# Kernel optimization log

Measured on AMD Instinct MI355X. Metric: run time of the kernel, lower is better.

The kernel has to match this reference:

```python
import jax, jax.numpy as jnp
import numpy as np

N = 50000
E = 800000
IN_C, HID, OUT_C, DEPTH, HEADS = 3, 128, 64, 4, 4
EPS = 1e-6
NEG_SLOPE = 0.2  # PyG GATConv default leaky_relu slope


def setup_inputs() -> dict:
    key = jax.random.key(0)
    ks = jax.random.split(key, 12)
    x = jax.random.normal(ks[0], (N, IN_C), dtype=jnp.float32)
    edge_index = jax.random.randint(ks[1], (2, E), 0, N, dtype=jnp.int32)
    s = 0.05
    return {
        "x": x,
        "edge_index": edge_index,
        "W_in": jax.random.normal(ks[2], (IN_C, HID), dtype=jnp.float32) * s,
        "b_in": jnp.zeros((HID,), jnp.float32),
        # per-layer GATConv params, stacked over depth
        "W_conv": jax.random.normal(ks[3], (DEPTH, HID, HEADS * HID), dtype=jnp.float32) * s,
        "att_src": jax.random.normal(ks[4], (DEPTH, HEADS, HID), dtype=jnp.float32) * s,
        "att_dst": jax.random.normal(ks[5], (DEPTH, HEADS, HID), dtype=jnp.float32) * s,
        "b_conv": jnp.zeros((DEPTH, HID), jnp.float32),
        "ln_gamma": jnp.ones((DEPTH, HID), jnp.float32),
        "ln_beta": jnp.zeros((DEPTH, HID), jnp.float32),
        "W_out": jax.random.normal(ks[6], (HID, OUT_C), dtype=jnp.float32) * s,
        "b_out": jnp.zeros((OUT_C,), jnp.float32),
    }


def _layer_norm(x, gamma, beta):
    mu = jnp.mean(x, axis=-1, keepdims=True)
    var = jnp.mean(jnp.square(x - mu), axis=-1, keepdims=True)
    return (x - mu) * jax.lax.rsqrt(var + EPS) * gamma + beta


def _gat_conv(x, src, dst, W, a_src, a_dst, bias):
    # x: [N, HID]; src/dst: [E2] (self-loops already appended)
    xh = (x @ W).reshape(N, HEADS, HID)                       # [N, H, C]
    alpha_s = jnp.einsum("nhc,hc->nh", xh, a_src)             # [N, H]
    alpha_d = jnp.einsum("nhc,hc->nh", xh, a_dst)             # [N, H]
    e = jax.nn.leaky_relu(alpha_s[src] + alpha_d[dst], NEG_SLOPE)  # [E2, H]
    # segment softmax over incoming edges of each destination node
    m = jax.ops.segment_max(e, dst, num_segments=N)           # [N, H]
    p = jnp.exp(e - m[dst])                                   # [E2, H]
    z = jax.ops.segment_sum(p, dst, num_segments=N)           # [N, H]
    alpha = p / z[dst]                                        # [E2, H]
    msg = alpha[:, :, None] * xh[src]                         # [E2, H, C]
    out = jax.ops.segment_sum(msg, dst, num_segments=N)       # [N, H, C]
    # concat=False -> mean over heads, then bias
    return out.mean(axis=1) + bias


def reference(x, edge_index, W_in, b_in, W_conv, att_src, att_dst, b_conv,
              ln_gamma, ln_beta, W_out, b_out):
    # add self-loops (PyG GATConv default add_self_loops=True)
    loops = jnp.arange(N, dtype=edge_index.dtype)
    src = jnp.concatenate([edge_index[0], loops])
    dst = jnp.concatenate([edge_index[1], loops])

    h = x @ W_in + b_in
    for i in range(DEPTH):
        residual = h
        h = _layer_norm(h, ln_gamma[i], ln_beta[i])
        h = _gat_conv(h, src, dst, W_conv[i], att_src[i], att_dst[i], b_conv[i])
        h = jax.nn.relu(h)
        h = h + residual
    return h @ W_out + b_out
```

## Files before the change

### kernel.cpp

```cpp
#include <hip/hip_runtime.h>
#include <hip/hip_fp16.h>
#include <math.h>

#define N_NODES 50000
#define E_EDGES 800000
#define E2 (E_EDGES + N_NODES)
#define HID 128
#define HEADS 4
#define OUTC 64
#define DEPTH 4
#define NEG_SLOPE 0.2f
#define LN_EPS 1e-6f
#define NT2 3125
#define AROW 520

typedef float f32x4 __attribute__((ext_vector_type(4)));
typedef float f32x2 __attribute__((ext_vector_type(2)));
typedef _Float16 half8 __attribute__((ext_vector_type(8)));


__global__ void k_deg(const int* __restrict__ ei, int* __restrict__ deg) {
    int e = blockIdx.x * 256 + threadIdx.x;
    if (e >= E2) return;
    int d = (e < E_EDGES) ? ei[E_EDGES + e] : (e - E_EDGES);
    atomicAdd(&deg[d], 1);
}


__global__ __launch_bounds__(256) void k_hist(const int* __restrict__ deg,
                                              int* __restrict__ hist) {
    __shared__ int lh[256];
    int t = threadIdx.x;
    lh[t] = 0;
    __syncthreads();
    int base = blockIdx.x * 1024;
    #pragma unroll
    for (int i = 0; i < 4; ++i) {
        int n = base + t + i * 256;
        if (n < N_NODES) atomicAdd(&lh[min(deg[n], 255)], 1);
    }
    __syncthreads();
    if (lh[t]) atomicAdd(&hist[t], lh[t]);
}


__global__ void k_hscan(const int* __restrict__ hist, int* __restrict__ hcur,
                        int* __restrict__ nprefix, int* __restrict__ eprefix,
                        int* __restrict__ row_ptr) {
    __shared__ int sm[256], se[256];
    int t = threadIdx.x;
    int v = hist[t];
    sm[t] = v;
    se[t] = v * t;
    __syncthreads();
    for (int off = 1; off < 256; off <<= 1) {
        int u = (t >= off) ? sm[t - off] : 0;
        int w = (t >= off) ? se[t - off] : 0;
        __syncthreads();
        sm[t] += u;
        se[t] += w;
        __syncthreads();
    }
    int np = sm[t] - v;
    int ep = se[t] - v * t;
    hcur[t] = np;
    nprefix[t] = np;
    eprefix[t] = ep;
    if (t == 0) row_ptr[N_NODES] = E2;
}


__global__ __launch_bounds__(256) void k_permfill(const int* __restrict__ deg,
                                                  int* __restrict__ hcur,
                                                  const int* __restrict__ nprefix,
                                                  const int* __restrict__ eprefix,
                                                  int* __restrict__ perm,
                                                  int* __restrict__ inv,
                                                  int* __restrict__ row_ptr) {
    __shared__ int lh[256];
    __shared__ int lbase[256];
    int t = threadIdx.x;
    lh[t] = 0;
    __syncthreads();
    int base = blockIdx.x * 1024;
    int myb[4], myr[4];
    #pragma unroll
    for (int i = 0; i < 4; ++i) {
        int n = base + t + i * 256;
        if (n < N_NODES) {
            int b = min(deg[n], 255);
            myb[i] = b;
            myr[i] = atomicAdd(&lh[b], 1);
        } else myb[i] = -1;
    }
    __syncthreads();
    if (lh[t]) lbase[t] = atomicAdd(&hcur[t], lh[t]);
    __syncthreads();
    #pragma unroll
    for (int i = 0; i < 4; ++i) {
        if (myb[i] >= 0) {
            int n = base + t + i * 256;
            int b = myb[i];
            int pos = lbase[b] + myr[i];
            perm[pos] = n;
            inv[n] = pos;
            row_ptr[pos] = eprefix[b] + (pos - nprefix[b]) * b;
        }
    }
}

__global__ void k_fill(const int* __restrict__ ei, const int* __restrict__ row_ptr,
                       const int* __restrict__ inv, int* __restrict__ cur,
                       int* __restrict__ csr_src) {
    int e = blockIdx.x * 256 + threadIdx.x;
    if (e >= E2) return;
    int s, d;
    if (e < E_EDGES) { s = ei[e]; d = ei[E_EDGES + e]; } else { s = d = e - E_EDGES; }
    int nd = inv[d], ns = inv[s];
    int pos = atomicAdd(&cur[nd], 1);
    csr_src[row_ptr[nd] + pos] = ns;
}


__global__ void k_prep(const float* __restrict__ W_conv, const float* __restrict__ att_s,
                       const float* __restrict__ att_d, const float* __restrict__ W_out,
                       _Float16* __restrict__ Bp, float* __restrict__ ws_all,
                       _Float16* __restrict__ Bout) {
    int idx = blockIdx.x * 256 + threadIdx.x;
    if (idx < DEPTH * 65536) {
        int jj    = idx & 7;
        int lane  = (idx >> 3) & 63;
        int kc    = (idx >> 9) & 15;
        int ntile = (idx >> 13) & 7;
        int layer = idx >> 16;
        int k = kc * 32 + (lane >> 4) * 8 + jj;
        int n = ntile * 16 + (lane & 15);
        int hh = k >> 7;
        int s  = k & 127;
        int c  = (s & 7) * 16 + (s >> 3);
        Bp[idx] = (_Float16)(0.25f * W_conv[(size_t)layer * 65536 + (size_t)c * 512 + hh * HID + n]);
        return;
    }
    int i2 = idx - DEPTH * 65536;
    if (i2 < DEPTH * 1024) {
        int j = i2 & 7, c = (i2 >> 3) & 127, layer = i2 >> 10;
        int hh = j & 3, sd = j >> 2;
        const float* Wr = W_conv + (size_t)layer * 65536 + (size_t)c * 512 + hh * HID;
        const float* at = (sd ? att_d : att_s) + (size_t)layer * HEADS * HID + hh * HID;
        float s = 0.f;
        for (int cc = 0; cc < HID; ++cc) s += Wr[cc] * at[cc];
        ws_all[i2] = s;
        return;
    }
    int i3 = i2 - DEPTH * 1024;
    if (i3 < 8192) {
        int j    = i3 & 7;
        int lane = (i3 >> 3) & 63;
        int nt   = (i3 >> 9) & 3;
        int kc   = i3 >> 11;
        int k = kc * 32 + (lane >> 4) * 8 + j;
        int c = (k & 7) * 16 + (k >> 3);
        int n = nt * 16 + (lane & 15);
        Bout[i3] = (_Float16)W_out[(size_t)c * OUTC + n];
    }
}


__global__ __launch_bounds__(256) void k_in_proj_ln(const float* __restrict__ x,
                                                    const int* __restrict__ perm,
                                                    const float* __restrict__ W,
                                                    const float* __restrict__ bias,
                                                    const float* __restrict__ gamma,
                                                    const float* __restrict__ beta,
                                                    const float* __restrict__ ws,
                                                    float* __restrict__ h,
                                                    unsigned char* __restrict__ ln8,
                                                    float* __restrict__ as_,
                                                    float* __restrict__ ad_) {
    int tid = threadIdx.x;
    int lane = tid & 63;
    int nd = blockIdx.x * 4 + (tid >> 6);
    int orig = perm[nd];
    const float* xr = x + (size_t)orig * 3;
    float x0 = xr[0], x1 = xr[1], x2 = xr[2];
    int j0 = lane, j1 = lane + 64;
    float a = bias[j0] + x0 * W[j0] + x1 * W[HID + j0] + x2 * W[2 * HID + j0];
    float b = bias[j1] + x0 * W[j1] + x1 * W[HID + j1] + x2 * W[2 * HID + j1];
    size_t base = (size_t)nd * HID;
    h[base + j0] = a;
    h[base + j1] = b;
    float s = a + b;
    for (int o = 1; o < 64; o <<= 1) s += __shfl_xor(s, o);
    float mu = s * (1.0f / 128.0f);
    float da = a - mu, db = b - mu;
    float v = da * da + db * db;
    for (int o = 1; o < 64; o <<= 1) v += __shfl_xor(v, o);
    float rstd = rsqrtf(v * (1.0f / 128.0f) + LN_EPS);
    float va = da * rstd * gamma[j0] + beta[j0];
    float vb = db * rstd * gamma[j1] + beta[j1];

    float ap[8];
    for (int j = 0; j < 8; ++j)
        ap[j] = va * ws[j0 * 8 + j] + vb * ws[j1 * 8 + j];
    for (int o = 1; o < 64; o <<= 1)
        for (int j = 0; j < 8; ++j) ap[j] += __shfl_xor(ap[j], o);
    if (lane == 0) {
        for (int hh = 0; hh < 4; ++hh) {
            as_[nd * 4 + hh] = ap[hh];
            ad_[nd * 4 + hh] = ap[4 + hh];
        }
    }

    float pv[8];
    for (int t = 0; t < 8; ++t) {
        int c = t * 16 + (lane & 15);
        float s1 = __shfl(va, c & 63);
        float s2 = __shfl(vb, c & 63);
        pv[t] = (c < 64) ? s1 : s2;
    }
    if (lane < 16) {
        int w0 = __builtin_amdgcn_cvt_pk_fp8_f32(pv[0], pv[1], 0, false);
        w0     = __builtin_amdgcn_cvt_pk_fp8_f32(pv[2], pv[3], w0, true);
        int w1 = __builtin_amdgcn_cvt_pk_fp8_f32(pv[4], pv[5], 0, false);
        w1     = __builtin_amdgcn_cvt_pk_fp8_f32(pv[6], pv[7], w1, true);
        *(int2*)(ln8 + base + lane * 8) = make_int2(w0, w1);
    }
}


__global__ __launch_bounds__(256, 4) void k_layer(const unsigned char* __restrict__ ln8r,
                                               const int* __restrict__ row_ptr,
                                               const int* __restrict__ csr_src,
                                               const float* __restrict__ asr,
                                               const float* __restrict__ adr,
                                               const _Float16* __restrict__ Bp,
                                               const float* __restrict__ ws,
                                               const float* __restrict__ bias,
                                               const float* __restrict__ gamma,
                                               const float* __restrict__ beta,
                                               float* __restrict__ h,
                                               unsigned char* __restrict__ ln8w,
                                               float* __restrict__ asw,
                                               float* __restrict__ adw,
                                               _Float16* __restrict__ h16,
                                               int write_ln, int last) {
    __shared__ __align__(16) unsigned char smraw[16 * AROW * 2];
    _Float16* Afr = (_Float16*)smraw;
    float (*Cts)[132] = (float (*)[132])smraw;

    int tid  = threadIdx.x;
    int lane = tid & 63;
    int w    = tid >> 6;
    int g    = lane >> 4;
    int l    = lane & 15;
    int quad = lane >> 4;
    int l15  = lane & 15;
    int tile = NT2 - 1 - blockIdx.x;
    int m    = w * 4 + g;
    int nd   = tile * 16 + m;

    int e0 = row_ptr[nd], e1 = row_ptr[nd + 1];
    float4 ad4 = *(const float4*)(adr + (size_t)nd * 4);

    f32x2 a00 = (f32x2)(0.f), a01 = (f32x2)(0.f), a02 = (f32x2)(0.f), a03 = (f32x2)(0.f);
    f32x2 a10 = (f32x2)(0.f), a11 = (f32x2)(0.f), a12 = (f32x2)(0.f), a13 = (f32x2)(0.f);
    f32x2 a20 = (f32x2)(0.f), a21 = (f32x2)(0.f), a22 = (f32x2)(0.f), a23 = (f32x2)(0.f);
    f32x2 a30 = (f32x2)(0.f), a31 = (f32x2)(0.f), a32 = (f32x2)(0.f), a33 = (f32x2)(0.f);
    float4 zz = make_float4(0.f, 0.f, 0.f, 0.f);

    const unsigned char* xb = ln8r + l * 8;

#define EDGE_P(Q, P) do {                                                   \
    float t_;                                                               \
    t_ = (Q).x + ad4.x; t_ = (t_ >= 0.f) ? t_ : NEG_SLOPE * t_; (P).x = __expf(t_); \
    t_ = (Q).y + ad4.y; t_ = (t_ >= 0.f) ? t_ : NEG_SLOPE * t_; (P).y = __expf(t_); \
    t_ = (Q).z + ad4.z; t_ = (t_ >= 0.f) ? t_ : NEG_SLOPE * t_; (P).z = __expf(t_); \
    t_ = (Q).w + ad4.w; t_ = (t_ >= 0.f) ? t_ : NEG_SLOPE * t_; (P).w = __expf(t_); \
} while (0)

#define ACC_EDGE(P, X) do {                                                 \
    f32x2 v0 = __builtin_amdgcn_cvt_pk_f32_fp8((X).x, false);               \
    f32x2 v1 = __builtin_amdgcn_cvt_pk_f32_fp8((X).x, true);                \
    f32x2 v2 = __builtin_amdgcn_cvt_pk_f32_fp8((X).y, false);               \
    f32x2 v3 = __builtin_amdgcn_cvt_pk_f32_fp8((X).y, true);                \
    a00 += (f32x2)((P).x) * v0; a01 += (f32x2)((P).x) * v1;                 \
    a02 += (f32x2)((P).x) * v2; a03 += (f32x2)((P).x) * v3;                 \
    a10 += (f32x2)((P).y) * v0; a11 += (f32x2)((P).y) * v1;                 \
    a12 += (f32x2)((P).y) * v2; a13 += (f32x2)((P).y) * v3;                 \
    a20 += (f32x2)((P).z) * v0; a21 += (f32x2)((P).z) * v1;                 \
    a22 += (f32x2)((P).z) * v2; a23 += (f32x2)((P).z) * v3;                 \
    a30 += (f32x2)((P).w) * v0; a31 += (f32x2)((P).w) * v1;                 \
    a32 += (f32x2)((P).w) * v2; a33 += (f32x2)((P).w) * v3;                 \
    zz.x += (P).x; zz.y += (P).y; zz.z += (P).z; zz.w += (P).w;             \
} while (0)

    int e = e0;
    for (; e + 4 <= e1; e += 4) {
        int s0 = csr_src[e];
        int s1 = csr_src[e + 1];
        int s2 = csr_src[e + 2];
        int s3 = csr_src[e + 3];
        float4 q0 = *(const float4*)(asr + (size_t)s0 * 4);
        float4 q1 = *(const float4*)(asr + (size_t)s1 * 4);
        float4 q2 = *(const float4*)(asr + (size_t)s2 * 4);
        float4 q3 = *(const float4*)(asr + (size_t)s3 * 4);
        int2 x0 = *(const int2*)(xb + (size_t)s0 * 128);
        int2 x1 = *(const int2*)(xb + (size_t)s1 * 128);
        int2 x2 = *(const int2*)(xb + (size_t)s2 * 128);
        int2 x3 = *(const int2*)(xb + (size_t)s3 * 128);
        float4 p0, p1, p2, p3;
        EDGE_P(q0, p0);
        EDGE_P(q1, p1);
        EDGE_P(q2, p2);
        EDGE_P(q3, p3);
        ACC_EDGE(p0, x0);
        ACC_EDGE(p1, x1);
        ACC_EDGE(p2, x2);
        ACC_EDGE(p3, x3);
    }
    for (; e < e1; ++e) {
        int s0 = csr_src[e];
        float4 q0 = *(const float4*)(asr + (size_t)s0 * 4);
        int2 x0 = *(const int2*)(xb + (size_t)s0 * 128);
        float4 p0;
        EDGE_P(q0, p0);
        ACC_EDGE(p0, x0);
    }
#undef EDGE_P
#undef ACC_EDGE

    {
        f32x2 i0 = (f32x2)(1.0f / zz.x), i1 = (f32x2)(1.0f / zz.y);
        f32x2 i2 = (f32x2)(1.0f / zz.z), i3 = (f32x2)(1.0f / zz.w);
        a00 *= i0; a01 *= i0; a02 *= i0; a03 *= i0;
        a10 *= i1; a11 *= i1; a12 *= i1; a13 *= i1;
        a20 *= i2; a21 *= i2; a22 *= i2; a23 *= i2;
        a30 *= i3; a31 *= i3; a32 *= i3; a33 *= i3;
        _Float16* rowp = Afr + m * AROW + l15 * 8;
        union { _Float16 hx[8]; int4 v4; } cf;
#define STORE_HEAD(H, P0, P1, P2, P3) do {                                  \
        cf.hx[0] = (_Float16)P0[0]; cf.hx[1] = (_Float16)P0[1];             \
        cf.hx[2] = (_Float16)P1[0]; cf.hx[3] = (_Float16)P1[1];             \
        cf.hx[4] = (_Float16)P2[0]; cf.hx[5] = (_Float16)P2[1];             \
        cf.hx[6] = (_Float16)P3[0]; cf.hx[7] = (_Float16)P3[1];             \
        *(int4*)(rowp + (H) * 128) = cf.v4;                                 \
} while (0)
        STORE_HEAD(0, a00, a01, a02, a03);
        STORE_HEAD(1, a10, a11, a12, a13);
        STORE_HEAD(2, a20, a21, a22, a23);
        STORE_HEAD(3, a30, a31, a32, a33);
#undef STORE_HEAD
    }
    __syncthreads();

    f32x4 c0 = (f32x4)(0.f), c1 = (f32x4)(0.f);
    {
        int nt0 = w * 2, nt1 = w * 2 + 1;
        const _Float16* b0p = Bp + (size_t)nt0 * 8192 + lane * 8;
        const _Float16* b1p = Bp + (size_t)nt1 * 8192 + lane * 8;
        const _Float16* ar = Afr + (lane & 15) * AROW + (lane >> 4) * 8;
        #pragma unroll
        for (int kc = 0; kc < 16; ++kc) {
            half8 a  = *(const half8*)(ar + kc * 32);
            half8 b0 = *(const half8*)(b0p + kc * 512);
            half8 b1 = *(const half8*)(b1p + kc * 512);
            c0 = __builtin_amdgcn_mfma_f32_16x16x32_f16(a, b0, c0, 0, 0, 0);
            c1 = __builtin_amdgcn_mfma_f32_16x16x32_f16(a, b1, c1, 0, 0, 0);
        }
    }
    __syncthreads();
    {
        int nt0 = w * 2, nt1 = w * 2 + 1;
        #pragma unroll
        for (int r = 0; r < 4; ++r) {
            Cts[quad * 4 + r][nt0 * 16 + l15] = c0[r];
            Cts[quad * 4 + r][nt1 * 16 + l15] = c1[r];
        }
    }
    __syncthreads();

    int row = quad * 4 + w;
    int node = tile * 16 + row;
    float* hr = h + (size_t)node * HID;

    float rv[8];
    #pragma unroll
    for (int nt = 0; nt < 8; ++nt) {
        float t = Cts[row][nt * 16 + l15] + bias[nt * 16 + l15];
        t = fmaxf(t, 0.f);
        rv[nt] = t + hr[nt * 16 + l15];
    }
    if (!last) {
        #pragma unroll
        for (int nt = 0; nt < 8; ++nt) hr[nt * 16 + l15] = rv[nt];
    } else {
        union { _Float16 hx[8]; int4 v4; } cf;
        #pragma unroll
        for (int nt = 0; nt < 8; ++nt) cf.hx[nt] = (_Float16)rv[nt];
        int kc = l15 >> 2;
        int lf = (l15 & 3) * 16 + row;
        *(int4*)(h16 + (((size_t)tile * 4 + kc) * 64 + lf) * 8) = cf.v4;
    }

    if (write_ln) {
        float ga[8], be[8];
        f32x4 wsa[8], wsb[8];
        #pragma unroll
        for (int nt = 0; nt < 8; ++nt) {
            int c = nt * 16 + l15;
            ga[nt] = gamma[c];
            be[nt] = beta[c];
            wsa[nt] = *(const f32x4*)(ws + c * 8);
            wsb[nt] = *(const f32x4*)(ws + c * 8 + 4);
        }
        float s = 0.f;
        #pragma unroll
        for (int nt = 0; nt < 8; ++nt) s += rv[nt];
        s += __shfl_xor(s, 1); s += __shfl_xor(s, 2);
        s += __shfl_xor(s, 4); s += __shfl_xor(s, 8);
        float mu = s * (1.0f / 128.0f);
        float var = 0.f;
        #pragma unroll
        for (int nt = 0; nt < 8; ++nt) { float d = rv[nt] - mu; var += d * d; }
        var += __shfl_xor(var, 1); var += __shfl_xor(var, 2);
        var += __shfl_xor(var, 4); var += __shfl_xor(var, 8);
        float rstd = rsqrtf(var * (1.0f / 128.0f) + LN_EPS);
        float lnv[8];
        #pragma unroll
        for (int nt = 0; nt < 8; ++nt)
            lnv[nt] = (rv[nt] - mu) * rstd * ga[nt] + be[nt];

        float ap[8];
        #pragma unroll
        for (int j = 0; j < 4; ++j) {
            float t0 = 0.f, t1 = 0.f;
            #pragma unroll
            for (int nt = 0; nt < 8; ++nt) {
                t0 += lnv[nt] * wsa[nt][j];
                t1 += lnv[nt] * wsb[nt][j];
            }
            ap[j] = t0;
            ap[4 + j] = t1;
        }
        #pragma unroll
        for (int j = 0; j < 8; ++j) {
            ap[j] += __shfl_xor(ap[j], 1); ap[j] += __shfl_xor(ap[j], 2);
            ap[j] += __shfl_xor(ap[j], 4); ap[j] += __shfl_xor(ap[j], 8);
        }
        if (l15 == 0) {
            for (int hh = 0; hh < 4; ++hh) {
                asw[node * 4 + hh] = ap[hh];
                adw[node * 4 + hh] = ap[4 + hh];
            }
        }

        int w0 = __builtin_amdgcn_cvt_pk_fp8_f32(lnv[0], lnv[1], 0, false);
        w0     = __builtin_amdgcn_cvt_pk_fp8_f32(lnv[2], lnv[3], w0, true);
        int w1 = __builtin_amdgcn_cvt_pk_fp8_f32(lnv[4], lnv[5], 0, false);
        w1     = __builtin_amdgcn_cvt_pk_fp8_f32(lnv[6], lnv[7], w1, true);
        *(int2*)(ln8w + (size_t)node * 128 + l15 * 8) = make_int2(w0, w1);
    }
}


__global__ __launch_bounds__(256) void k_out_proj_mfma(const _Float16* __restrict__ h16,
                                                       const _Float16* __restrict__ Bout,
                                                       const int* __restrict__ perm,
                                                       const float* __restrict__ b,
                                                       float* __restrict__ out) {
    int tid = threadIdx.x;
    int lane = tid & 63;
    int tile = blockIdx.x * 4 + (tid >> 6);
    if (tile >= NT2) return;

    const _Float16* ab = h16 + (size_t)tile * 2048 + lane * 8;
    f32x4 acc[4];
    for (int nt = 0; nt < 4; ++nt) acc[nt] = (f32x4)(0.0f);
    #pragma unroll
    for (int kc = 0; kc < 4; ++kc) {
        half8 a = *(const half8*)(ab + kc * 512);
        #pragma unroll
        for (int nt = 0; nt < 4; ++nt) {
            half8 bf = *(const half8*)(Bout + ((size_t)(kc * 4 + nt) * 64 + lane) * 8);
            acc[nt] = __builtin_amdgcn_mfma_f32_16x16x32_f16(a, bf, acc[nt], 0, 0, 0);
        }
    }

    int l15 = lane & 15, quad = lane >> 4;
    float bo[4];
    #pragma unroll
    for (int nt = 0; nt < 4; ++nt) bo[nt] = b[nt * 16 + l15];
    #pragma unroll
    for (int r = 0; r < 4; ++r) {
        int node = perm[tile * 16 + quad * 4 + r];
        float* orow = out + (size_t)node * OUTC;
        #pragma unroll
        for (int nt = 0; nt < 4; ++nt)
            orow[nt * 16 + l15] = acc[nt][r] + bo[nt];
    }
}


extern "C" void kernel_launch(void* const* d_in, const int* in_sizes, int n_in,
                              void* d_out, int out_size, void* d_ws, size_t ws_size,
                              hipStream_t stream) {
    const float* x       = (const float*)d_in[0];
    const int*   ei      = (const int*)d_in[1];
    const float* W_in    = (const float*)d_in[2];
    const float* b_in    = (const float*)d_in[3];
    const float* W_conv  = (const float*)d_in[4];
    const float* att_src = (const float*)d_in[5];
    const float* att_dst = (const float*)d_in[6];
    const float* b_conv  = (const float*)d_in[7];
    const float* ln_g    = (const float*)d_in[8];
    const float* ln_b    = (const float*)d_in[9];
    const float* W_out   = (const float*)d_in[10];
    const float* b_out   = (const float*)d_in[11];
    float* out = (float*)d_out;

    char* ws = (char*)d_ws;
    size_t off = 0;
    auto alloc = [&](size_t bytes) { void* p = ws + off; off = (off + bytes + 255) & ~(size_t)255; return p; };
    float* h            = (float*)alloc((size_t)N_NODES * HID * 4);
    unsigned char* ln8a = (unsigned char*)alloc((size_t)N_NODES * 128);
    unsigned char* ln8b = (unsigned char*)alloc((size_t)N_NODES * 128);
    float* asa          = (float*)alloc((size_t)N_NODES * 4 * 4);
    float* asb          = (float*)alloc((size_t)N_NODES * 4 * 4);
    float* ada          = (float*)alloc((size_t)N_NODES * 4 * 4);
    float* adb          = (float*)alloc((size_t)N_NODES * 4 * 4);
    _Float16* Bp2       = (_Float16*)alloc((size_t)DEPTH * 65536 * 2);
    float* ws_all       = (float*)alloc((size_t)DEPTH * 1024 * 4);
    _Float16* h16       = (_Float16*)alloc((size_t)NT2 * 2048 * 2);
    _Float16* Bout      = (_Float16*)alloc((size_t)8192 * 2);
    int* deg    = (int*)alloc((size_t)N_NODES * 4);
    int* cur    = (int*)alloc((size_t)N_NODES * 4);
    int* hist   = (int*)alloc(256 * 4);
    int* row_ptr= (int*)alloc((size_t)(N_NODES + 1) * 4);
    int* csr    = (int*)alloc((size_t)E2 * 4);
    int* perm   = (int*)alloc((size_t)N_NODES * 4);
    int* inv    = (int*)alloc((size_t)N_NODES * 4);
    int* hcur   = (int*)alloc(256 * 4);
    int* nprefix= (int*)alloc(256 * 4);
    int* eprefix= (int*)alloc(256 * 4);
    (void)ws_size; (void)n_in; (void)in_sizes; (void)out_size;

    size_t zspan = (char*)(hist + 256) - (char*)deg;
    hipMemsetAsync(deg, 0, zspan, stream);

    k_deg<<<(E2 + 255) / 256, 256, 0, stream>>>(ei, deg);
    int nbh = (N_NODES + 1023) / 1024;
    k_hist<<<nbh, 256, 0, stream>>>(deg, hist);
    k_hscan<<<1, 256, 0, stream>>>(hist, hcur, nprefix, eprefix, row_ptr);
    k_permfill<<<nbh, 256, 0, stream>>>(deg, hcur, nprefix, eprefix, perm, inv, row_ptr);
    k_fill<<<(E2 + 255) / 256, 256, 0, stream>>>(ei, row_ptr, inv, cur, csr);

    int prep_total = DEPTH * 65536 + DEPTH * 1024 + 8192;
    k_prep<<<(prep_total + 255) / 256, 256, 0, stream>>>(W_conv, att_src, att_dst, W_out,
                                                         Bp2, ws_all, Bout);

    k_in_proj_ln<<<N_NODES / 4, 256, 0, stream>>>(x, perm, W_in, b_in, ln_g, ln_b, ws_all,
                                                  h, ln8a, asa, ada);

    for (int i = 0; i < DEPTH; ++i) {
        const float* bcp = b_conv + (size_t)i * HID;
        int write_ln = (i + 1 < DEPTH) ? 1 : 0;
        int last = (i + 1 == DEPTH) ? 1 : 0;
        int nl = (i + 1 < DEPTH) ? i + 1 : i;
        const float* gp = ln_g + (size_t)nl * HID;
        const float* bp = ln_b + (size_t)nl * HID;
        const float* wsp = ws_all + (size_t)nl * 1024;

        const unsigned char* l8r = (i & 1) ? ln8b : ln8a;
        unsigned char*       l8w = (i & 1) ? ln8a : ln8b;
        const float* asr = (i & 1) ? asb : asa;
        float*       asw = (i & 1) ? asa : asb;
        const float* adr = (i & 1) ? adb : ada;
        float*       adw = (i & 1) ? ada : adb;

        k_layer<<<NT2, 256, 0, stream>>>(l8r, row_ptr, csr, asr, adr,
                                         Bp2 + (size_t)i * 65536, wsp,
                                         bcp, gp, bp, h, l8w, asw, adw,
                                         h16, write_ln, last);
    }

    k_out_proj_mfma<<<(NT2 + 3) / 4, 256, 0, stream>>>(h16, Bout, perm, b_out, out);
}
```

Measured before the change: 426.3 us.

## Distribute per-edge softmax exp across lanes and double-buffer edge gathers

In the fused GAT aggregation kernel, each of the 16 lanes in a node group now computes a single (edge, head) attention exponent instead of every lane redundantly computing all four heads for four edges. The results are broadcast with shuffles, and the softmax denominator is reduced across lanes at the end. Edge-chunk loads are double-buffered (A/B register sets) so gathers for the next chunk are issued before the current chunk is accumulated. Tile order is also changed from reversed to forward. The change trades redundant exp/leaky-relu work for extra shuffle traffic and higher register pressure, which could lower occupancy.

```diff
diff --git a/kernel.cpp b/kernel.cpp
--- a/kernel.cpp
+++ b/kernel.cpp
@@ -255,28 +255,26 @@
     int l    = lane & 15;
     int quad = lane >> 4;
     int l15  = lane & 15;
-    int tile = NT2 - 1 - blockIdx.x;
+    int tile = blockIdx.x;
     int m    = w * 4 + g;
     int nd   = tile * 16 + m;
 
     int e0 = row_ptr[nd], e1 = row_ptr[nd + 1];
     float4 ad4 = *(const float4*)(adr + (size_t)nd * 4);
+
+    int gb = lane & 0x30;
+    int jj = (lane >> 2) & 3;
+    int hh = lane & 3;
+    float adh = (hh == 0) ? ad4.x : (hh == 1) ? ad4.y : (hh == 2) ? ad4.z : ad4.w;
 
     f32x2 a00 = (f32x2)(0.f), a01 = (f32x2)(0.f), a02 = (f32x2)(0.f), a03 = (f32x2)(0.f);
     f32x2 a10 = (f32x2)(0.f), a11 = (f32x2)(0.f), a12 = (f32x2)(0.f), a13 = (f32x2)(0.f);
     f32x2 a20 = (f32x2)(0.f), a21 = (f32x2)(0.f), a22 = (f32x2)(0.f), a23 = (f32x2)(0.f);
     f32x2 a30 = (f32x2)(0.f), a31 = (f32x2)(0.f), a32 = (f32x2)(0.f), a33 = (f32x2)(0.f);
-    float4 zz = make_float4(0.f, 0.f, 0.f, 0.f);
+    float z_own = 0.f;
+    float4 zt = make_float4(0.f, 0.f, 0.f, 0.f);
 
     const unsigned char* xb = ln8r + l * 8;
-
-#define EDGE_P(Q, P) do {                                                   \
-    float t_;                                                               \
-    t_ = (Q).x + ad4.x; t_ = (t_ >= 0.f) ? t_ : NEG_SLOPE * t_; (P).x = __expf(t_); \
-    t_ = (Q).y + ad4.y; t_ = (t_ >= 0.f) ? t_ : NEG_SLOPE * t_; (P).y = __expf(t_); \
-    t_ = (Q).z + ad4.z; t_ = (t_ >= 0.f) ? t_ : NEG_SLOPE * t_; (P).z = __expf(t_); \
-    t_ = (Q).w + ad4.w; t_ = (t_ >= 0.f) ? t_ : NEG_SLOPE * t_; (P).w = __expf(t_); \
-} while (0)
 
 #define ACC_EDGE(P, X) do {                                                 \
     f32x2 v0 = __builtin_amdgcn_cvt_pk_f32_fp8((X).x, false);               \
@@ -291,43 +289,104 @@
     a22 += (f32x2)((P).z) * v2; a23 += (f32x2)((P).z) * v3;                 \
     a30 += (f32x2)((P).w) * v0; a31 += (f32x2)((P).w) * v1;                 \
     a32 += (f32x2)((P).w) * v2; a33 += (f32x2)((P).w) * v3;                 \
-    zz.x += (P).x; zz.y += (P).y; zz.z += (P).z; zz.w += (P).w;             \
 } while (0)
 
-    int e = e0;
-    for (; e + 4 <= e1; e += 4) {
-        int s0 = csr_src[e];
-        int s1 = csr_src[e + 1];
-        int s2 = csr_src[e + 2];
-        int s3 = csr_src[e + 3];
-        float4 q0 = *(const float4*)(asr + (size_t)s0 * 4);
-        float4 q1 = *(const float4*)(asr + (size_t)s1 * 4);
-        float4 q2 = *(const float4*)(asr + (size_t)s2 * 4);
-        float4 q3 = *(const float4*)(asr + (size_t)s3 * 4);
-        int2 x0 = *(const int2*)(xb + (size_t)s0 * 128);
-        int2 x1 = *(const int2*)(xb + (size_t)s1 * 128);
-        int2 x2 = *(const int2*)(xb + (size_t)s2 * 128);
-        int2 x3 = *(const int2*)(xb + (size_t)s3 * 128);
-        float4 p0, p1, p2, p3;
-        EDGE_P(q0, p0);
-        EDGE_P(q1, p1);
-        EDGE_P(q2, p2);
-        EDGE_P(q3, p3);
-        ACC_EDGE(p0, x0);
-        ACC_EDGE(p1, x1);
-        ACC_EDGE(p2, x2);
-        ACC_EDGE(p3, x3);
-    }
-    for (; e < e1; ++e) {
+    int sA0, sA1, sA2, sA3, sB0, sB1, sB2, sB3;
+    float qA, qB;
+    int2 xA0, xA1, xA2, xA3, xB0, xB1, xB2, xB3;
+
+#define LOADC(S, be) do {                                                   \
+    sS##S##0 = csr_src[(be)];     sS##S##1 = csr_src[(be) + 1];             \
+    sS##S##2 = csr_src[(be) + 2]; sS##S##3 = csr_src[(be) + 3];             \
+    int sel_ = (jj == 0) ? sS##S##0 : (jj == 1) ? sS##S##1                  \
+             : (jj == 2) ? sS##S##2 : sS##S##3;                             \
+    q##S = asr[(size_t)sel_ * 4 + hh];                                      \
+    x##S##0 = *(const int2*)(xb + (size_t)sS##S##0 * 128);                  \
+    x##S##1 = *(const int2*)(xb + (size_t)sS##S##1 * 128);                  \
+    x##S##2 = *(const int2*)(xb + (size_t)sS##S##2 * 128);                  \
+    x##S##3 = *(const int2*)(xb + (size_t)sS##S##3 * 128);                  \
+} while (0)
+#define sSA0 sA0
+#define sSA1 sA1
+#define sSA2 sA2
+#define sSA3 sA3
+#define sSB0 sB0
+#define sSB1 sB1
+#define sSB2 sB2
+#define sSB3 sB3
+
+#define COMPUTEC(S) do {                                                    \
+    float t_ = q##S + adh;                                                  \
+    t_ = (t_ >= 0.f) ? t_ : NEG_SLOPE * t_;                                 \
+    float p_ = __expf(t_);                                                  \
+    z_own += p_;                                                            \
+    float4 pp;                                                              \
+    pp.x = __shfl(p_, gb + 0);  pp.y = __shfl(p_, gb + 1);                  \
+    pp.z = __shfl(p_, gb + 2);  pp.w = __shfl(p_, gb + 3);                  \
+    ACC_EDGE(pp, x##S##0);                                                  \
+    pp.x = __shfl(p_, gb + 4);  pp.y = __shfl(p_, gb + 5);                  \
+    pp.z = __shfl(p_, gb + 6);  pp.w = __shfl(p_, gb + 7);                  \
+    ACC_EDGE(pp, x##S##1);                                                  \
+    pp.x = __shfl(p_, gb + 8);  pp.y = __shfl(p_, gb + 9);                  \
+    pp.z = __shfl(p_, gb + 10); pp.w = __shfl(p_, gb + 11);                 \
+    ACC_EDGE(pp, x##S##2);                                                  \
+    pp.x = __shfl(p_, gb + 12); pp.y = __shfl(p_, gb + 13);                 \
+    pp.z = __shfl(p_, gb + 14); pp.w = __shfl(p_, gb + 15);                 \
+    ACC_EDGE(pp, x##S##3);                                                  \
+} while (0)
+
+    int nc = (e1 - e0) >> 2;
+    if (nc >= 2) {
+        LOADC(A, e0);
+        LOADC(B, e0 + 4);
+        int c = 2;
+        int eb = e0 + 8;
+        for (; c + 1 < nc; c += 2) {
+            COMPUTEC(A);
+            LOADC(A, eb);
+            COMPUTEC(B);
+            LOADC(B, eb + 4);
+            eb += 8;
+        }
+        if (c < nc) {
+            COMPUTEC(A);
+            LOADC(A, eb);
+            COMPUTEC(B);
+            COMPUTEC(A);
+        } else {
+            COMPUTEC(A);
+            COMPUTEC(B);
+        }
+    } else if (nc == 1) {
+        LOADC(A, e0);
+        COMPUTEC(A);
+    }
+
+    for (int e = e0 + nc * 4; e < e1; ++e) {
         int s0 = csr_src[e];
         float4 q0 = *(const float4*)(asr + (size_t)s0 * 4);
         int2 x0 = *(const int2*)(xb + (size_t)s0 * 128);
         float4 p0;
-        EDGE_P(q0, p0);
+        float t_;
+        t_ = q0.x + ad4.x; t_ = (t_ >= 0.f) ? t_ : NEG_SLOPE * t_; p0.x = __expf(t_);
+        t_ = q0.y + ad4.y; t_ = (t_ >= 0.f) ? t_ : NEG_SLOPE * t_; p0.y = __expf(t_);
+        t_ = q0.z + ad4.z; t_ = (t_ >= 0.f) ? t_ : NEG_SLOPE * t_; p0.z = __expf(t_);
+        t_ = q0.w + ad4.w; t_ = (t_ >= 0.f) ? t_ : NEG_SLOPE * t_; p0.w = __expf(t_);
         ACC_EDGE(p0, x0);
-    }
-#undef EDGE_P
+        zt.x += p0.x; zt.y += p0.y; zt.z += p0.z; zt.w += p0.w;
+    }
 #undef ACC_EDGE
+#undef LOADC
+#undef COMPUTEC
+
+    float zr = z_own;
+    zr += __shfl_xor(zr, 4);
+    zr += __shfl_xor(zr, 8);
+    float4 zz;
+    zz.x = __shfl(zr, gb + 0) + zt.x;
+    zz.y = __shfl(zr, gb + 1) + zt.y;
+    zz.z = __shfl(zr, gb + 2) + zt.z;
+    zz.w = __shfl(zr, gb + 3) + zt.w;
 
     {
         f32x2 i0 = (f32x2)(1.0f / zz.x), i1 = (f32x2)(1.0f / zz.y);
@@ -448,9 +507,9 @@
             ap[j] += __shfl_xor(ap[j], 4); ap[j] += __shfl_xor(ap[j], 8);
         }
         if (l15 == 0) {
-            for (int hh = 0; hh < 4; ++hh) {
-                asw[node * 4 + hh] = ap[hh];
-                adw[node * 4 + hh] = ap[4 + hh];
+            for (int hh2 = 0; hh2 < 4; ++hh2) {
+                asw[node * 4 + hh2] = ap[hh2];
+                adw[node * 4 + hh2] = ap[4 + hh2];
             }
         }
 
```

Result: slower. 541.1 us (+26.9%).
